# Optimization experiments

Hardware: AMD Instinct MI355X
Metric: run time of the kernel (lower is better)

The kernel has to match this reference:

```python
import jax, jax.numpy as jnp
import numpy as np

B, S, H, NH = 2, 2048, 2048, 32
HD = H // NH  # 64

def _causal_mask(b, s, dtype=jnp.float32):
    neg = jnp.finfo(dtype).min
    m = jnp.where(jnp.tril(jnp.ones((s, s), dtype=bool)), 0.0, neg).astype(dtype)
    return jnp.broadcast_to(m[None, None], (b, 1, s, s))

def setup_inputs() -> dict:
    key = jax.random.key(0)
    k1, k2, k3, k4, k5 = jax.random.split(key, 5)
    scale = 1.0 / np.sqrt(H)
    return {
        "hidden_states": jax.random.normal(k1, (B, S, H), jnp.float32),
        "attention_mask": _causal_mask(B, S),
        "Wq": jax.random.normal(k2, (H, H), jnp.float32) * scale,
        "Wk": jax.random.normal(k3, (H, H), jnp.float32) * scale,
        "Wv": jax.random.normal(k4, (H, H), jnp.float32) * scale,
        "Wo": jax.random.normal(k5, (H, H), jnp.float32) * scale,
    }

def reference(hidden_states, attention_mask, Wq, Wk, Wv, Wo):
    b, s, _ = hidden_states.shape
    dt = hidden_states.dtype
    def proj(W):  # torch Linear: x @ W.T -> [b, nh, s, hd]
        return (hidden_states @ W.T).reshape(b, s, NH, HD).transpose(0, 2, 1, 3)
    q, k, v = proj(Wq), proj(Wk), proj(Wv)
    attn = jnp.einsum('bhqd,bhkd->bhqk', q, k) / np.sqrt(HD)
    attn = attn + attention_mask
    attn = jnp.maximum(attn, jnp.finfo(attn.dtype).min)
    attn = jax.nn.softmax(attn.astype(jnp.float32), axis=-1).astype(dt)
    out = jnp.einsum('bhqk,bhkd->bhqd', attn, v)
    out = out.transpose(0, 2, 1, 3).reshape(b, s, H)
    return out @ Wo.T
```

## Files before the change

kernel.cpp:

```cpp
#include <hip/hip_runtime.h>
#include <hip/hip_bf16.h>
#include <stdint.h>

#define S_LEN 2048
#define NHEAD 32
#define HDIM  64

using bf16x8 = __attribute__((ext_vector_type(8))) short;
using f32x4  = __attribute__((ext_vector_type(4))) float;
using f32x16 = __attribute__((ext_vector_type(16))) float;

__device__ __forceinline__ uint16_t f2bf(float f) {
  union { float f; uint32_t u; } c; c.f = f;
  uint32_t u = c.u;
  return (uint16_t)((u + 0x7FFFu + ((u >> 16) & 1u)) >> 16);
}

__device__ __forceinline__ void load_lds16(const void* g, void* l) {
  __builtin_amdgcn_global_load_lds(
      (const __attribute__((address_space(1))) void*)g,
      (__attribute__((address_space(3))) void*)l, 16, 0, 0);
}

__device__ __forceinline__ f32x16 mfma32(bf16x8 a, bf16x8 b, f32x16 c) {
  return __builtin_amdgcn_mfma_f32_32x32x16_bf16(a, b, c, 0, 0, 0);
}

__device__ __forceinline__ uint32_t cvtpk(float lo, float hi_) {
  uint32_t d;
  asm("v_cvt_pk_bf16_f32 %0, %1, %2" : "=v"(d) : "v"(lo), "v"(hi_));
  return d;
}
__device__ __forceinline__ void plswap(uint32_t& a, uint32_t& b) {
  asm volatile("v_permlane32_swap_b32 %0, %1" : "+v"(a), "+v"(b));
}

__global__ __launch_bounds__(256) void conv_batch(
    const float* __restrict__ X, const float* __restrict__ Wq,
    const float* __restrict__ Wk, const float* __restrict__ Wv,
    uint16_t* __restrict__ Xbf, uint16_t* __restrict__ Wqk,
    uint16_t* __restrict__ Wvb) {
  int i = blockIdx.x * 256 + threadIdx.x;
  const float* src; uint16_t* dst; int o;
  if (i < 2097152)      { src = X;  dst = Xbf;           o = i; }
  else if (i < 3145728) { src = Wq; dst = Wqk;           o = i - 2097152; }
  else if (i < 4194304) { src = Wk; dst = Wqk + 4194304; o = i - 3145728; }
  else                  { src = Wv; dst = Wvb;           o = i - 4194304; }
  float4 v = ((const float4*)src)[o];
  uint64_t packed = (uint64_t)f2bf(v.x) | ((uint64_t)f2bf(v.y) << 16) |
                    ((uint64_t)f2bf(v.z) << 32) | ((uint64_t)f2bf(v.w) << 48);
  ((uint64_t*)dst)[o] = packed;
}

__global__ __launch_bounds__(256) void conv_f32_bf16(
    const float* __restrict__ in, uint16_t* __restrict__ out, int n4) {
  int i = blockIdx.x * 256 + threadIdx.x;
  if (i < n4) {
    float4 v = ((const float4*)in)[i];
    uint64_t packed = (uint64_t)f2bf(v.x) | ((uint64_t)f2bf(v.y) << 16) |
                      ((uint64_t)f2bf(v.z) << 32) | ((uint64_t)f2bf(v.w) << 48);
    ((uint64_t*)out)[i] = packed;
  }
}

__global__ __launch_bounds__(512, 2) void gemm_qk(
    const uint16_t* __restrict__ A, const uint16_t* __restrict__ Bw,
    uint16_t* __restrict__ Qo, uint16_t* __restrict__ Ko, float qscale) {
  extern __shared__ char smem[];
  const int t = threadIdx.x;
  const int lane = t & 63, w = t >> 6;
  const int lrow = lane & 15, lgrp = lane >> 4;
  const int wr = w >> 2, wc = w & 3;
  const int id = blockIdx.x;
  const int swz = (id & 7) * 32 + (id >> 3);
  const int bm = (swz & 15) * 256, bn = (swz >> 4) * 256;
  constexpr int NT = 2048 / 32;

  const f32x4 zero4 = {0.f, 0.f, 0.f, 0.f};
  f32x4 acc[8][4];
#pragma unroll
  for (int mi = 0; mi < 8; ++mi)
#pragma unroll
    for (int ni = 0; ni < 4; ++ni) acc[mi][ni] = zero4;

  auto stage_mat = [&](const uint16_t* __restrict__ G, int grow0,
                       char* ldsbase, int kt) {
#pragma unroll
    for (int j = 0; j < 2; ++j) {
      const int s = t + j * 512;
      const int row = s >> 2;
      const int sc = (s & 3) ^ ((row >> 1) & 3);
      load_lds16(G + (size_t)(grow0 + row) * 2048 + kt + sc * 8,
                 ldsbase + j * 8192 + w * 1024);
    }
  };
  auto lda = [&](const char* Ab, int mi) -> bf16x8 {
    const int row = wr * 128 + mi * 16 + lrow;
    return *(const bf16x8*)(Ab + row * 64 + ((lgrp ^ ((row >> 1) & 3)) << 4));
  };
  auto ldb = [&](const char* Bb, int ni) -> bf16x8 {
    const int row = wc * 64 + ni * 16 + lrow;
    return *(const bf16x8*)(Bb + row * 64 + ((lgrp ^ ((row >> 1) & 3)) << 4));
  };

  stage_mat(A, bm, smem, 0);
  stage_mat(Bw, bn, smem + 16384, 0);
  stage_mat(A, bm, smem + 32768, 32);
  stage_mat(Bw, bn, smem + 32768 + 16384, 32);

  for (int kt = 0; kt < NT; ++kt) {
    char* cur = smem + (kt % 3) * 32768;
    if (kt < NT - 1) asm volatile("s_waitcnt vmcnt(4)" ::: "memory");
    else             asm volatile("s_waitcnt vmcnt(0)" ::: "memory");
    __builtin_amdgcn_s_barrier();

    if (kt + 2 < NT) {
      char* nx2 = smem + ((kt + 2) % 3) * 32768;
      stage_mat(A, bm, nx2, (kt + 2) * 32);
      stage_mat(Bw, bn, nx2 + 16384, (kt + 2) * 32);
    }

    bf16x8 aF[8], bF[4];
#pragma unroll
    for (int mi = 0; mi < 8; ++mi) aF[mi] = lda(cur, mi);
#pragma unroll
    for (int ni = 0; ni < 4; ++ni) bF[ni] = ldb(cur + 16384, ni);
#pragma unroll
    for (int mi = 0; mi < 8; ++mi)
#pragma unroll
      for (int ni = 0; ni < 4; ++ni)
        acc[mi][ni] = __builtin_amdgcn_mfma_f32_16x16x32_bf16(
            aF[mi], bF[ni], acc[mi][ni], 0, 0, 0);
  }

  const bool isQ = (bn < 2048);
#pragma unroll
  for (int mi = 0; mi < 8; ++mi) {
#pragma unroll
    for (int ni = 0; ni < 4; ++ni) {
      const int n = bn + wc * 64 + ni * 16 + lrow;
      const int n2 = isQ ? n : (n - 2048);
      const int h = n2 >> 6, d = n2 & 63;
#pragma unroll
      for (int r = 0; r < 4; ++r) {
        const int m = bm + wr * 128 + mi * 16 + lgrp * 4 + r;
        const int b = m >> 11, s = m & 2047;
        const size_t off = (((size_t)(b * NHEAD + h) * S_LEN + s) * HDIM) + d;
        if (isQ) Qo[off] = f2bf(acc[mi][ni][r] * qscale);
        else     Ko[off] = f2bf(acc[mi][ni][r]);
      }
    }
  }
}

template<int MODE>
__global__ __launch_bounds__(256, 3) void gemm_nt(
    const uint16_t* __restrict__ A, const uint16_t* __restrict__ B,
    void* __restrict__ C, int M, int N, int K, float scale) {
  __shared__ __align__(16) char smem[3][16384];

  const int t = threadIdx.x;
  const int lane = t & 63, w = t >> 6;
  const int lrow = lane & 15, lgrp = lane >> 4;
  const int bm = blockIdx.y * 128, bn = blockIdx.x * 128;
  const int wm = (w >> 1) * 64, wn = (w & 1) * 64;
  const int NT = K / 32;

  const f32x4 zero4 = {0.f, 0.f, 0.f, 0.f};
  f32x4 acc[4][4];
#pragma unroll
  for (int mi = 0; mi < 4; ++mi)
#pragma unroll
    for (int ni = 0; ni < 4; ++ni) acc[mi][ni] = zero4;

  auto stage_mat = [&](const uint16_t* __restrict__ G, int grow0,
                       char* ldsbase, int kt) {
#pragma unroll
    for (int j = 0; j < 2; ++j) {
      const int s = t + j * 256;
      const int row = s >> 2;
      const int sc = (s & 3) ^ ((row >> 1) & 3);
      load_lds16(G + (size_t)(grow0 + row) * K + kt + sc * 8,
                 ldsbase + j * 4096 + w * 1024);
    }
  };
  auto ldf = [&](const char* Mb, int base, int i) -> bf16x8 {
    const int row = base + i * 16 + lrow;
    return *(const bf16x8*)(Mb + row * 64 + ((lgrp ^ ((row >> 1) & 3)) << 4));
  };

  stage_mat(A, bm, smem[0], 0);
  stage_mat(B, bn, smem[0] + 8192, 0);
  stage_mat(A, bm, smem[1], 32);
  stage_mat(B, bn, smem[1] + 8192, 32);

  for (int kt = 0; kt < NT; ++kt) {
    char* cur = smem[kt % 3];
    if (kt < NT - 1) asm volatile("s_waitcnt vmcnt(4)" ::: "memory");
    else             asm volatile("s_waitcnt vmcnt(0)" ::: "memory");
    __builtin_amdgcn_s_barrier();

    if (kt + 2 < NT) {
      char* nx2 = smem[(kt + 2) % 3];
      stage_mat(A, bm, nx2, (kt + 2) * 32);
      stage_mat(B, bn, nx2 + 8192, (kt + 2) * 32);
    }

    bf16x8 aF[4], bF[4];
#pragma unroll
    for (int mi = 0; mi < 4; ++mi) aF[mi] = ldf(cur, wm, mi);
#pragma unroll
    for (int ni = 0; ni < 4; ++ni) bF[ni] = ldf(cur + 8192, wn, ni);
#pragma unroll
    for (int mi = 0; mi < 4; ++mi)
#pragma unroll
      for (int ni = 0; ni < 4; ++ni)
        acc[mi][ni] = __builtin_amdgcn_mfma_f32_16x16x32_bf16(
            aF[mi], bF[ni], acc[mi][ni], 0, 0, 0);
  }

#pragma unroll
  for (int mi = 0; mi < 4; ++mi) {
#pragma unroll
    for (int ni = 0; ni < 4; ++ni) {
      const int n = bn + wn + ni * 16 + lrow;
#pragma unroll
      for (int r = 0; r < 4; ++r) {
        const int m = bm + wm + mi * 16 + lgrp * 4 + r;
        const float v = acc[mi][ni][r] * scale;
        if (MODE == 2) {
          ((float*)C)[(size_t)m * N + n] = v;
        } else {
          const int h = m >> 6, d = m & 63;
          const int b = n >> 11, s = n & 2047;
          ((uint16_t*)C)[(((size_t)(b * NHEAD + h) * HDIM + d) * S_LEN) + s] =
              f2bf(v);
        }
      }
    }
  }
}

__global__ __launch_bounds__(256, 3) void attn_kernel(
    const uint16_t* __restrict__ Q, const uint16_t* __restrict__ K,
    const uint16_t* __restrict__ Vt, uint16_t* __restrict__ O) {
  __shared__ __align__(16) uint16_t Ks[2][64 * 64];
  __shared__ __align__(16) uint16_t Vs[2][64 * 64];
  __shared__ float Ls[4][32];

  const int t = threadIdx.x, lane = t & 63, w = t >> 6;
  const int qcol = lane & 31, hi = lane >> 5;
  const int id = blockIdx.x;
  const int bh = (id & 7) * 8 + ((id >> 3) & 7);
  const int p = id >> 6;
  const int b = bh >> 5, h = bh & 31;

  const uint16_t* Qbh = Q + (size_t)bh * S_LEN * HDIM;
  const uint16_t* Kbh = K + (size_t)bh * S_LEN * HDIM;
  const uint16_t* Vbh = Vt + (size_t)bh * HDIM * S_LEN;

  const int srow = lane >> 3;
  const int schunk = (lane & 7) ^ srow;

  auto stage = [&](int k0, int bi) {
#pragma unroll
    for (int j = 0; j < 2; ++j) {
      const int r = j * 32 + w * 8 + srow;
      load_lds16(Kbh + (size_t)(k0 + r) * HDIM + schunk * 8,
                 (char*)&Ks[bi][0] + j * 4096 + w * 1024);
      load_lds16(Vbh + (size_t)r * S_LEN + k0 + schunk * 8,
                 (char*)&Vs[bi][0] + j * 4096 + w * 1024);
    }
  };

  for (int pass = 0; pass < 2; ++pass) {
    const int jq = pass ? (15 - p) : p;
    const int qw = jq * 128 + w * 32;
    const int qg = qw + qcol;

    bf16x8 qB[4];
    {
      const uint16_t* qp = Qbh + (size_t)(qw + qcol) * HDIM + hi * 8;
#pragma unroll
      for (int j = 0; j < 4; ++j) qB[j] = *(const bf16x8*)(qp + 16 * j);
    }

    f32x16 oacc0, oacc1;
#pragma unroll
    for (int r = 0; r < 16; ++r) { oacc0[r] = 0.f; oacc1[r] = 0.f; }
    float lsum = 0.f;

    const int nt = 2 * jq + 2;
    for (int kt = 0; kt < nt; ++kt) {
      const int cur = kt & 1;
      const int k0 = kt * 64;
      if (kt == 0) { __syncthreads(); stage(0, 0); }
      __syncthreads();
      if (kt + 1 < nt) stage((kt + 1) * 64, cur ^ 1);

      if (k0 <= qw + 31) {
        const char* Kc = (const char*)&Ks[cur][0];
        const char* Vc = (const char*)&Vs[cur][0];

        f32x16 s0, s1;
#pragma unroll
        for (int r = 0; r < 16; ++r) { s0[r] = 0.f; s1[r] = 0.f; }
        const int rk0 = qcol, rk1 = 32 + qcol;
        const int x0 = rk0 & 7;
        __builtin_amdgcn_s_setprio(1);
#pragma unroll
        for (int j = 0; j < 4; ++j) {
          bf16x8 kf0 = *(const bf16x8*)(Kc + rk0 * 128 + (((2*j+hi) ^ x0) << 4));
          bf16x8 kf1 = *(const bf16x8*)(Kc + rk1 * 128 + (((2*j+hi) ^ x0) << 4));
          s0 = mfma32(kf0, qB[j], s0);
          s1 = mfma32(kf1, qB[j], s1);
        }
        __builtin_amdgcn_s_setprio(0);

        if (k0 + 63 > qw) {
#pragma unroll
          for (int r = 0; r < 16; ++r) {
            const int krow = (r & 3) + 8 * (r >> 2) + 4 * hi;
            s0[r] = (k0 + krow <= qg) ? __expf(s0[r]) : 0.f;
            s1[r] = (k0 + 32 + krow <= qg) ? __expf(s1[r]) : 0.f;
            lsum += s0[r] + s1[r];
          }
        } else {
#pragma unroll
          for (int r = 0; r < 16; ++r) {
            s0[r] = __expf(s0[r]);
            s1[r] = __expf(s1[r]);
            lsum += s0[r] + s1[r];
          }
        }

        bf16x8 paf[4];
#pragma unroll
        for (int tt = 0; tt < 4; ++tt) {
          const int o = 8 * (tt & 1);
          uint32_t a0, a1, a2, a3;
          if (tt < 2) {
            a0 = cvtpk(s0[o + 0], s0[o + 1]);
            a1 = cvtpk(s0[o + 2], s0[o + 3]);
            a2 = cvtpk(s0[o + 4], s0[o + 5]);
            a3 = cvtpk(s0[o + 6], s0[o + 7]);
          } else {
            a0 = cvtpk(s1[o + 0], s1[o + 1]);
            a1 = cvtpk(s1[o + 2], s1[o + 3]);
            a2 = cvtpk(s1[o + 4], s1[o + 5]);
            a3 = cvtpk(s1[o + 6], s1[o + 7]);
          }
          plswap(a0, a2);
          plswap(a1, a3);
          union { uint32_t u[4]; bf16x8 v; } pk;
          pk.u[0] = a0; pk.u[1] = a1; pk.u[2] = a2; pk.u[3] = a3;
          paf[tt] = pk.v;
        }

        __builtin_amdgcn_s_setprio(1);
#pragma unroll
        for (int tt = 0; tt < 4; ++tt) {
          const int c = 2 * tt + hi;
          bf16x8 v0f = *(const bf16x8*)(Vc + rk0 * 128 + ((c ^ x0) << 4));
          bf16x8 v1f = *(const bf16x8*)(Vc + rk1 * 128 + ((c ^ x0) << 4));
          oacc0 = mfma32(paf[tt], v0f, oacc0);
          oacc1 = mfma32(paf[tt], v1f, oacc1);
        }
        __builtin_amdgcn_s_setprio(0);
      }
    }

    lsum += __shfl_xor(lsum, 32, 64);
    if (hi == 0) Ls[w][qcol] = 1.0f / lsum;

#pragma unroll
    for (int r = 0; r < 16; ++r) {
      const int qrow = (r & 3) + 8 * (r >> 2) + 4 * hi;
      const float inv = Ls[w][qrow];
      const size_t base = ((size_t)b * S_LEN + qw + qrow) * 2048 + h * 64;
      O[base + qcol] = f2bf(oacc0[r] * inv);
      O[base + 32 + qcol] = f2bf(oacc1[r] * inv);
    }
  }
}

extern "C" void kernel_launch(void* const* d_in, const int* in_sizes, int n_in,
                              void* d_out, int out_size, void* d_ws,
                              size_t ws_size, hipStream_t stream) {
  const float* X  = (const float*)d_in[0];
  const float* Wq = (const float*)d_in[2];
  const float* Wk = (const float*)d_in[3];
  const float* Wv = (const float*)d_in[4];
  const float* Wo = (const float*)d_in[5];
  float* out = (float*)d_out;

  char* ws = (char*)d_ws;
  uint16_t* Xbf = (uint16_t*)ws;
  uint16_t* Wqk = (uint16_t*)(ws + 16777216);
  uint16_t* Qb  = (uint16_t*)(ws + 33554432);
  uint16_t* Kb  = (uint16_t*)(ws + 50331648);
  uint16_t* Wsm = (uint16_t*)(ws + 67108864);
  uint16_t* Vtb = Wqk;
  uint16_t* Ob  = Xbf;

  const float qscale = 0.125f;

  hipFuncSetAttribute((const void*)gemm_qk,
                      hipFuncAttributeMaxDynamicSharedMemorySize, 98304);

  conv_batch<<<20480, 256, 0, stream>>>(X, Wq, Wk, Wv, Xbf, Wqk, Wsm);
  gemm_qk<<<256, 512, 98304, stream>>>(Xbf, Wqk, Qb, Kb, qscale);
  gemm_nt<1><<<dim3(32, 16), 256, 0, stream>>>(Wsm, Xbf, Vtb, 2048, 4096, 2048, 1.0f);
  attn_kernel<<<dim3(512), 256, 0, stream>>>(Qb, Kb, Vtb, Ob);
  conv_f32_bf16<<<4096, 256, 0, stream>>>(Wo, Wsm, 1048576);
  gemm_nt<2><<<dim3(16, 32), 256, 0, stream>>>(Ob, Wsm, out, 4096, 2048, 2048, 1.0f);
}
```

Before: 233.5 us.

## Retile QK projection GEMM to 256x128 tiles with double-buffered static LDS

Changes the fused Q/K projection GEMM from 512-thread blocks over 256x256 tiles with a 3-stage 96KB dynamic LDS ring to 256-thread blocks over 256x128 tiles with a 2-stage 48KB static LDS buffer. It also remaps blocks so each XCD gets a contiguous band of N columns, and it adds a second barrier before refilling the buffer just consumed. The goal is more blocks (512), lower LDS use per block and better occupancy and L2 locality. The cost is more A-matrix reloads, since B tiles are narrower, plus an extra barrier per k-step that shortens the prefetch distance.

```diff
diff --git a/kernel.cpp b/kernel.cpp
--- a/kernel.cpp
+++ b/kernel.cpp
@@ -63,17 +63,18 @@
   }
 }
 
-__global__ __launch_bounds__(512, 2) void gemm_qk(
+__global__ __launch_bounds__(256, 2) void gemm_qk(
     const uint16_t* __restrict__ A, const uint16_t* __restrict__ Bw,
     uint16_t* __restrict__ Qo, uint16_t* __restrict__ Ko, float qscale) {
-  extern __shared__ char smem[];
+  __shared__ __align__(16) char smem[2][24576];
   const int t = threadIdx.x;
   const int lane = t & 63, w = t >> 6;
   const int lrow = lane & 15, lgrp = lane >> 4;
-  const int wr = w >> 2, wc = w & 3;
+  const int wm = (w >> 1) * 128, wn = (w & 1) * 64;
   const int id = blockIdx.x;
-  const int swz = (id & 7) * 32 + (id >> 3);
-  const int bm = (swz & 15) * 256, bn = (swz >> 4) * 256;
+  const int xcd = id & 7, loc = id >> 3;
+  const int bm = (loc & 15) * 256;
+  const int bn = (xcd * 4 + (loc >> 4)) * 128;
   constexpr int NT = 2048 / 32;
 
   const f32x4 zero4 = {0.f, 0.f, 0.f, 0.f};
@@ -83,54 +84,53 @@
 #pragma unroll
     for (int ni = 0; ni < 4; ++ni) acc[mi][ni] = zero4;
 
-  auto stage_mat = [&](const uint16_t* __restrict__ G, int grow0,
-                       char* ldsbase, int kt) {
-#pragma unroll
-    for (int j = 0; j < 2; ++j) {
-      const int s = t + j * 512;
+  auto stage = [&](char* buf, int kt) {
+#pragma unroll
+    for (int j = 0; j < 4; ++j) {
+      const int s = t + j * 256;
       const int row = s >> 2;
       const int sc = (s & 3) ^ ((row >> 1) & 3);
-      load_lds16(G + (size_t)(grow0 + row) * 2048 + kt + sc * 8,
-                 ldsbase + j * 8192 + w * 1024);
+      load_lds16(A + (size_t)(bm + row) * 2048 + kt + sc * 8,
+                 buf + j * 4096 + w * 1024);
+    }
+#pragma unroll
+    for (int j = 0; j < 2; ++j) {
+      const int s = t + j * 256;
+      const int row = s >> 2;
+      const int sc = (s & 3) ^ ((row >> 1) & 3);
+      load_lds16(Bw + (size_t)(bn + row) * 2048 + kt + sc * 8,
+                 buf + 16384 + j * 4096 + w * 1024);
     }
   };
-  auto lda = [&](const char* Ab, int mi) -> bf16x8 {
-    const int row = wr * 128 + mi * 16 + lrow;
-    return *(const bf16x8*)(Ab + row * 64 + ((lgrp ^ ((row >> 1) & 3)) << 4));
+  auto ldf = [&](const char* base, int roff, int i) -> bf16x8 {
+    const int row = roff + i * 16 + lrow;
+    return *(const bf16x8*)(base + row * 64 +
+                            ((lgrp ^ ((row >> 1) & 3)) << 4));
   };
-  auto ldb = [&](const char* Bb, int ni) -> bf16x8 {
-    const int row = wc * 64 + ni * 16 + lrow;
-    return *(const bf16x8*)(Bb + row * 64 + ((lgrp ^ ((row >> 1) & 3)) << 4));
-  };
-
-  stage_mat(A, bm, smem, 0);
-  stage_mat(Bw, bn, smem + 16384, 0);
-  stage_mat(A, bm, smem + 32768, 32);
-  stage_mat(Bw, bn, smem + 32768 + 16384, 32);
+
+  stage(smem[0], 0);
+  stage(smem[1], 32);
 
   for (int kt = 0; kt < NT; ++kt) {
-    char* cur = smem + (kt % 3) * 32768;
-    if (kt < NT - 1) asm volatile("s_waitcnt vmcnt(4)" ::: "memory");
+    char* cur = smem[kt & 1];
+    if (kt < NT - 1) asm volatile("s_waitcnt vmcnt(6)" ::: "memory");
     else             asm volatile("s_waitcnt vmcnt(0)" ::: "memory");
     __builtin_amdgcn_s_barrier();
 
-    if (kt + 2 < NT) {
-      char* nx2 = smem + ((kt + 2) % 3) * 32768;
-      stage_mat(A, bm, nx2, (kt + 2) * 32);
-      stage_mat(Bw, bn, nx2 + 16384, (kt + 2) * 32);
-    }
-
     bf16x8 aF[8], bF[4];
 #pragma unroll
-    for (int mi = 0; mi < 8; ++mi) aF[mi] = lda(cur, mi);
-#pragma unroll
-    for (int ni = 0; ni < 4; ++ni) bF[ni] = ldb(cur + 16384, ni);
+    for (int mi = 0; mi < 8; ++mi) aF[mi] = ldf(cur, wm, mi);
+#pragma unroll
+    for (int ni = 0; ni < 4; ++ni) bF[ni] = ldf(cur + 16384, wn, ni);
 #pragma unroll
     for (int mi = 0; mi < 8; ++mi)
 #pragma unroll
       for (int ni = 0; ni < 4; ++ni)
         acc[mi][ni] = __builtin_amdgcn_mfma_f32_16x16x32_bf16(
             aF[mi], bF[ni], acc[mi][ni], 0, 0, 0);
+
+    __builtin_amdgcn_s_barrier();
+    if (kt + 2 < NT) stage(cur, (kt + 2) * 32);
   }
 
   const bool isQ = (bn < 2048);
@@ -138,12 +138,12 @@
   for (int mi = 0; mi < 8; ++mi) {
 #pragma unroll
     for (int ni = 0; ni < 4; ++ni) {
-      const int n = bn + wc * 64 + ni * 16 + lrow;
+      const int n = bn + wn + ni * 16 + lrow;
       const int n2 = isQ ? n : (n - 2048);
       const int h = n2 >> 6, d = n2 & 63;
 #pragma unroll
       for (int r = 0; r < 4; ++r) {
-        const int m = bm + wr * 128 + mi * 16 + lgrp * 4 + r;
+        const int m = bm + wm + mi * 16 + lgrp * 4 + r;
         const int b = m >> 11, s = m & 2047;
         const size_t off = (((size_t)(b * NHEAD + h) * S_LEN + s) * HDIM) + d;
         if (isQ) Qo[off] = f2bf(acc[mi][ni][r] * qscale);
@@ -405,11 +405,8 @@
 
   const float qscale = 0.125f;
 
-  hipFuncSetAttribute((const void*)gemm_qk,
-                      hipFuncAttributeMaxDynamicSharedMemorySize, 98304);
-
   conv_batch<<<20480, 256, 0, stream>>>(X, Wq, Wk, Wv, Xbf, Wqk, Wsm);
-  gemm_qk<<<256, 512, 98304, stream>>>(Xbf, Wqk, Qb, Kb, qscale);
+  gemm_qk<<<512, 256, 0, stream>>>(Xbf, Wqk, Qb, Kb, qscale);
   gemm_nt<1><<<dim3(32, 16), 256, 0, stream>>>(Wsm, Xbf, Vtb, 2048, 4096, 2048, 1.0f);
   attn_kernel<<<dim3(512), 256, 0, stream>>>(Qb, Kb, Vtb, Ob);
   conv_f32_bf16<<<4096, 256, 0, stream>>>(Wo, Wsm, 1048576);
```

New measurement: 237.7 us. Within noise of the previous version (+1.8%).
